# Optimization experiments

Measured on AMD Instinct MI355X. Metric: run time of the kernel, lower is better.

## Reference

```python
import jax, jax.numpy as jnp
import numpy as np

N_SRC = 1024     # source frames
N_TGT = 100000   # target pool frames
D = 1024         # WavLM layer-6 feature dim
K = 4            # neighbors


def setup_inputs() -> dict:
    key = jax.random.key(0)
    k1, k2 = jax.random.split(key)
    source_feats = jax.random.normal(k1, (N_SRC, D), dtype=jnp.float32)
    target_feats = jax.random.normal(k2, (N_TGT, D), dtype=jnp.float32)
    return {"source_feats": source_feats, "target_feats": target_feats, "k": K}


def reference(source_feats, target_feats, k):
    # Cosine distance kNN: smallest cosine distance == largest cosine similarity.
    s = source_feats / jnp.linalg.norm(source_feats, axis=-1, keepdims=True)
    t = target_feats / jnp.linalg.norm(target_feats, axis=-1, keepdims=True)
    sim = jnp.einsum('nd,md->nm', s, t)          # [N_SRC, N_TGT]
    _, idx = jax.lax.top_k(sim, k)               # [N_SRC, k] neighbor indices
    # Gather ORIGINAL (un-normalized) target rows and average over neighbors,
    # matching sklearn kneighbors + target_np[indices].mean(axis=0).
    gathered = target_feats[idx]                 # [N_SRC, k, D]
    return gathered.mean(axis=1)                 # [N_SRC, D]
```

## Files before the change

### kernel.cpp

```cpp
#include <hip/hip_runtime.h>
#include <hip/hip_bf16.h>
#include <float.h>

#define N_SRC 1024
#define N_TGT 100000
#define DIM   1024
#define KNN   4

#define BM 128
#define BN 256
#define BK 64
#define NKT (DIM / BK)
#define NMB 782
#define N_TGT2 (NMB * BM)
#define NSC (N_SRC / BN)
#define NBLK (NMB * NSC)
#define NSTRIP NMB
#define NCAND (NSTRIP * KNN)
#define RERANK 32

#define SRC_KT_B 65536ull
#define TGT_KT_B ((unsigned long long)N_TGT2 * 64ull)

typedef __attribute__((ext_vector_type(4))) float f32x4;
typedef __attribute__((ext_vector_type(4))) unsigned int u32x4;
typedef __attribute__((ext_vector_type(2))) long long i64x2;

__device__ __forceinline__ void gload16(const void* gp, void* lp) {
    __builtin_amdgcn_global_load_lds(
        (const __attribute__((address_space(1))) void*)gp,
        (__attribute__((address_space(3))) void*)lp, 16, 0, 0);
}

__device__ __forceinline__ unsigned int pk_fp8x4(float x0, float x1,
                                                 float x2, float x3) {
    int d = __builtin_amdgcn_cvt_pk_fp8_f32(x0, x1, 0, false);
    d     = __builtin_amdgcn_cvt_pk_fp8_f32(x2, x3, d, true);
    return (unsigned int)d;
}

__device__ __forceinline__ void ce_desc(float& v1, int& i1, float& v2, int& i2)
{
    bool sw = (v2 > v1) || (v2 == v1 && i2 < i1);
    float tv = sw ? v2 : v1; float uv = sw ? v1 : v2;
    int   ti = sw ? i2 : i1; int   ui = sw ? i1 : i2;
    v1 = tv; i1 = ti; v2 = uv; i2 = ui;
}

__global__ __launch_bounds__(256) void convert_src_kernel(
    const float* __restrict__ src, unsigned int* __restrict__ srcws)
{
    int gid = blockIdx.x * 256 + threadIdx.x;
    int kt  = gid >> 12;
    int rem = gid & 4095;
    int row = rem >> 2;
    int pos = rem & 3;
    int c   = pos ^ ((row >> 1) & 3);
    const float4* p0 = (const float4*)(src + (size_t)row * DIM + kt * BK + c * 8);
    const float4* p1 = (const float4*)(src + (size_t)row * DIM + kt * BK + 32 + c * 8);
    float4 a0 = p0[0], a1 = p0[1], b0 = p1[0], b1 = p1[1];
    u32x4 o = { pk_fp8x4(a0.x, a0.y, a0.z, a0.w),
                pk_fp8x4(a1.x, a1.y, a1.z, a1.w),
                pk_fp8x4(b0.x, b0.y, b0.z, b0.w),
                pk_fp8x4(b1.x, b1.y, b1.z, b1.w) };
    ((u32x4*)srcws)[gid] = o;
}

__global__ __launch_bounds__(256) void prep_tgt_kernel(
    const float* __restrict__ tgt, unsigned int* __restrict__ tgtbf,
    float* __restrict__ invnw)
{
    __shared__ float pn[16][17];
    const int t  = threadIdx.x;
    const int li = t & 15;
    const int kt = t >> 4;
    const int row = blockIdx.x * 16 + li;
    const bool valid = row < N_TGT;

    float4 v[16];
    if (valid) {
        const float4* p = (const float4*)(tgt + (size_t)row * DIM + kt * BK);
        #pragma unroll
        for (int i = 0; i < 16; ++i) v[i] = p[i];
    } else {
        #pragma unroll
        for (int i = 0; i < 16; ++i) v[i] = make_float4(0.f, 0.f, 0.f, 0.f);
    }
    float nsq = 0.f;
    #pragma unroll
    for (int i = 0; i < 16; ++i)
        nsq += v[i].x * v[i].x + v[i].y * v[i].y
             + v[i].z * v[i].z + v[i].w * v[i].w;

    u32x4* o = (u32x4*)((char*)tgtbf + (size_t)kt * TGT_KT_B
                        + (size_t)row * 64);
    const int f = (row >> 1) & 3;
    #pragma unroll
    for (int c = 0; c < 4; ++c) {
        float4 a0 = v[2 * c], a1 = v[2 * c + 1];
        float4 b0 = v[8 + 2 * c], b1 = v[8 + 2 * c + 1];
        o[c ^ f] = (u32x4){ pk_fp8x4(a0.x, a0.y, a0.z, a0.w),
                            pk_fp8x4(a1.x, a1.y, a1.z, a1.w),
                            pk_fp8x4(b0.x, b0.y, b0.z, b0.w),
                            pk_fp8x4(b1.x, b1.y, b1.z, b1.w) };
    }

    pn[li][kt] = nsq;
    __syncthreads();
    if (t < 16) {
        float s = 0.f;
        #pragma unroll
        for (int k = 0; k < 16; ++k) s += pn[t][k];
        int r2 = blockIdx.x * 16 + t;
        invnw[r2] = (r2 < N_TGT) ? 1.0f / sqrtf(s) : -1.0f;
    }
}

__global__ __launch_bounds__(512, 4) void gemm_topk_fp8_kernel(
    const void* __restrict__ tgtbf, const void* __restrict__ srcbf,
    const float* __restrict__ invnw,
    float* __restrict__ cand_val, int* __restrict__ cand_idx)
{
    __shared__ __align__(16) unsigned char As[2][BM][BK];
    __shared__ __align__(16) unsigned char Bs[2][BN][BK];
    __shared__ float invn_sh[BM];

    const int b = blockIdx.x;
    const int logical = (b & 7) * (NBLK / 8) + (b >> 3);
    const int mblk = logical >> 2;
    const int schk = logical & 3;
    const int m0 = mblk * BM;
    const int c0 = schk * BN;

    const int t = threadIdx.x;
    const int lane = t & 63;
    const int w = t >> 6;
    const int wm = w >> 2, wn = w & 3;
    const int g = lane >> 4, li = lane & 15;

    const char* tb_ = (const char*)tgtbf;
    const char* sb_ = (const char*)srcbf;

    f32x4 acc[4][4];
    #pragma unroll
    for (int i = 0; i < 4; ++i)
        #pragma unroll
        for (int j = 0; j < 4; ++j) acc[i][j] = (f32x4){0.f, 0.f, 0.f, 0.f};

    unsigned char *Ac = &As[0][0][0], *An = &As[1][0][0];
    unsigned char *Bc = &Bs[0][0][0], *Bn = &Bs[1][0][0];

    #define STAGE(Ab_, Bb_, kt_) do {                                         \
        const char* ga_ = tb_ + (size_t)(kt_) * TGT_KT_B + (size_t)m0 * 64    \
                          + (size_t)t * 16;                                   \
        gload16(ga_, (Ab_) + t * 16);                                         \
        const char* gb_ = sb_ + (size_t)(kt_) * SRC_KT_B + (size_t)c0 * 64    \
                          + (size_t)t * 16;                                   \
        gload16(gb_,        (Bb_) + t * 16);                                  \
        gload16(gb_ + 8192, (Bb_) + 8192 + t * 16);                           \
    } while (0)

    const int sl = (g ^ ((li >> 1) & 3)) * 16;

    #define READ_AB do {                                                      \
        _Pragma("unroll")                                                     \
        for (int mf = 0; mf < 4; ++mf)                                        \
            af[mf] = *(const i64x2*)(Ac + (wm * 64 + mf * 16 + li) * BK + sl);\
        _Pragma("unroll")                                                     \
        for (int nf = 0; nf < 4; ++nf)                                        \
            bf[nf] = *(const i64x2*)(Bc + (wn * 64 + nf * 16 + li) * BK + sl);\
    } while (0)

    #define DO_MFMA do {                                                      \
        _Pragma("unroll")                                                     \
        for (int mf = 0; mf < 4; ++mf)                                        \
            _Pragma("unroll")                                                 \
            for (int nf = 0; nf < 4; ++nf)                                    \
                acc[mf][nf] = __builtin_amdgcn_mfma_f32_16x16x32_fp8_fp8(     \
                    af[mf][0], bf[nf][0], acc[mf][nf], 0, 0, 0);              \
        _Pragma("unroll")                                                     \
        for (int mf = 0; mf < 4; ++mf)                                        \
            _Pragma("unroll")                                                 \
            for (int nf = 0; nf < 4; ++nf)                                    \
                acc[mf][nf] = __builtin_amdgcn_mfma_f32_16x16x32_fp8_fp8(     \
                    af[mf][1], bf[nf][1], acc[mf][nf], 0, 0, 0);              \
    } while (0)

    STAGE(Ac, Bc, 0);
    __syncthreads();

    for (int kt = 0; kt < NKT; ++kt) {
        if (kt + 1 < NKT) STAGE(An, Bn, kt + 1);
        i64x2 af[4], bf[4];
        READ_AB;
        DO_MFMA;
        __syncthreads();
        unsigned char* tmp_;
        tmp_ = Ac; Ac = An; An = tmp_;
        tmp_ = Bc; Bc = Bn; Bn = tmp_;
    }
    #undef STAGE
    #undef READ_AB
    #undef DO_MFMA

    float* scv = (float*)&As[0][0][0];
    int*   sci = (int*)&As[1][0][0];

    if (t < BM) invn_sh[t] = invnw[m0 + t];
    __syncthreads();

    float invr[4][4];
    #pragma unroll
    for (int mf = 0; mf < 4; ++mf)
        #pragma unroll
        for (int j = 0; j < 4; ++j)
            invr[mf][j] = invn_sh[wm * 64 + mf * 16 + g * 4 + j];

    #pragma unroll
    for (int nf = 0; nf < 4; ++nf) {
        const int col = wn * 64 + nf * 16 + li;
        float s[4][4];
        #pragma unroll
        for (int mf = 0; mf < 4; ++mf)
            #pragma unroll
            for (int j = 0; j < 4; ++j)
                s[mf][j] = (invr[mf][j] > 0.f) ? acc[mf][nf][j] * invr[mf][j]
                                               : -FLT_MAX;
        #pragma unroll
        for (int it = 0; it < KNN; ++it) {
            float bv = -FLT_MAX; int bli = 0;
            #pragma unroll
            for (int mf = 0; mf < 4; ++mf)
                #pragma unroll
                for (int j = 0; j < 4; ++j) {
                    int id = mf * 16 + g * 4 + j;
                    if (s[mf][j] > bv) { bv = s[mf][j]; bli = id; }
                }
            #pragma unroll
            for (int off = 16; off < 64; off <<= 1) {
                float ov = __shfl_xor(bv, off);
                int   oi = __shfl_xor(bli, off);
                if (ov > bv || (ov == bv && oi < bli)) { bv = ov; bli = oi; }
            }
            const int mfw = bli >> 4, gw = (bli >> 2) & 3, jw = bli & 3;
            if (g == gw) {
                #pragma unroll
                for (int mf = 0; mf < 4; ++mf)
                    #pragma unroll
                    for (int j = 0; j < 4; ++j)
                        if (mf == mfw && j == jw) s[mf][j] = -FLT_MAX;
            }
            if (g == it) {
                int o = (wm * BN + col) * KNN + it;
                scv[o] = bv;
                sci[o] = m0 + wm * 64 + bli;
            }
        }
    }
    __syncthreads();

    if (t < BN) {
        float v4[4] = { -FLT_MAX, -FLT_MAX, -FLT_MAX, -FLT_MAX };
        int   i4[4] = { 0x7fffffff, 0x7fffffff, 0x7fffffff, 0x7fffffff };
        #pragma unroll
        for (int q = 0; q < 8; ++q) {
            int o = ((q >> 2) * BN + t) * KNN + (q & 3);
            float v = scv[o]; int ix = sci[o];
            if (v > v4[3] || (v == v4[3] && ix < i4[3])) {
                v4[3] = v; i4[3] = ix;
                ce_desc(v4[2], i4[2], v4[3], i4[3]);
                ce_desc(v4[1], i4[1], v4[2], i4[2]);
                ce_desc(v4[0], i4[0], v4[1], i4[1]);
            }
        }
        size_t o = ((size_t)(c0 + t) * NSTRIP + mblk) * KNN;
        #pragma unroll
        for (int it = 0; it < KNN; ++it) {
            cand_val[o + it] = v4[it];
            cand_idx[o + it] = i4[it];
        }
    }
}

__global__ __launch_bounds__(256) void merge_rerank_kernel(
    const float* __restrict__ src, const float* __restrict__ tgt,
    const float* __restrict__ cand_val, const int* __restrict__ cand_idx,
    float* __restrict__ out)
{
    __shared__ float sv[NCAND];
    __shared__ float red_v[4];
    __shared__ int   red_p[4];
    __shared__ int   topi[RERANK];
    __shared__ float rsim[RERANK];
    __shared__ int   ridx[RERANK];
    __shared__ int   sel[KNN];

    const int row = blockIdx.x;
    const int t = threadIdx.x, lane = t & 63, w = t >> 6;
    const float* cv = cand_val + (size_t)row * NCAND;
    const int*   ci = cand_idx + (size_t)row * NCAND;

    for (int i = t; i < NCAND; i += 256) sv[i] = cv[i];
    __syncthreads();

    for (int it = 0; it < RERANK; ++it) {
        float bv = -FLT_MAX; int bp = 0;
        for (int i = t; i < NCAND; i += 256) {
            float v = sv[i];
            if (v > bv) { bv = v; bp = i; }
        }
        #pragma unroll
        for (int off = 1; off < 64; off <<= 1) {
            float ov = __shfl_xor(bv, off);
            int   op = __shfl_xor(bp, off);
            if (ov > bv || (ov == bv && op < bp)) { bv = ov; bp = op; }
        }
        if (lane == 0) { red_v[w] = bv; red_p[w] = bp; }
        __syncthreads();
        if (t == 0) {
            float Bv = red_v[0]; int Bp = red_p[0];
            for (int q = 1; q < 4; ++q)
                if (red_v[q] > Bv || (red_v[q] == Bv && red_p[q] < Bp)) {
                    Bv = red_v[q]; Bp = red_p[q];
                }
            topi[it] = ci[Bp];
            sv[Bp] = -FLT_MAX;
        }
        __syncthreads();
    }

    const float4* sp = (const float4*)(src + (size_t)row * DIM);
    #pragma unroll
    for (int q = 0; q < 8; ++q) {
        int cidx = topi[w + 4 * q];
        const float4* tp = (const float4*)(tgt + (size_t)cidx * DIM);
        float a = 0.f, nn = 0.f;
        #pragma unroll
        for (int p = 0; p < 4; ++p) {
            float4 x = sp[lane + 64 * p], y = tp[lane + 64 * p];
            a  = fmaf(x.x, y.x, a);  a  = fmaf(x.y, y.y, a);
            a  = fmaf(x.z, y.z, a);  a  = fmaf(x.w, y.w, a);
            nn = fmaf(y.x, y.x, nn); nn = fmaf(y.y, y.y, nn);
            nn = fmaf(y.z, y.z, nn); nn = fmaf(y.w, y.w, nn);
        }
        #pragma unroll
        for (int off = 1; off < 64; off <<= 1) {
            a  += __shfl_xor(a, off);
            nn += __shfl_xor(nn, off);
        }
        if (lane == 0) { rsim[w + 4 * q] = a / sqrtf(nn); ridx[w + 4 * q] = cidx; }
    }
    __syncthreads();

    if (w == 0) {
        float v = (lane < RERANK) ? rsim[lane] : -FLT_MAX;
        int  ix = (lane < RERANK) ? ridx[lane] : 0x7fffffff;
        #pragma unroll
        for (int it = 0; it < KNN; ++it) {
            float bv = v; int bix = ix;
            #pragma unroll
            for (int off = 1; off < 32; off <<= 1) {
                float ov = __shfl_xor(bv, off);
                int   oi = __shfl_xor(bix, off);
                if (ov > bv || (ov == bv && oi < bix)) { bv = ov; bix = oi; }
            }
            if (lane == 0) sel[it] = bix;
            if (ix == bix) v = -FLT_MAX;
        }
    }
    __syncthreads();

    const float4* g0 = (const float4*)(tgt + (size_t)sel[0] * DIM);
    const float4* g1 = (const float4*)(tgt + (size_t)sel[1] * DIM);
    const float4* g2 = (const float4*)(tgt + (size_t)sel[2] * DIM);
    const float4* g3 = (const float4*)(tgt + (size_t)sel[3] * DIM);
    float4* po = (float4*)(out + (size_t)row * DIM);
    float4 v0 = g0[t], v1 = g1[t], v2 = g2[t], v3 = g3[t];
    float4 rr;
    rr.x = (v0.x + v1.x + v2.x + v3.x) * 0.25f;
    rr.y = (v0.y + v1.y + v2.y + v3.y) * 0.25f;
    rr.z = (v0.z + v1.z + v2.z + v3.z) * 0.25f;
    rr.w = (v0.w + v1.w + v2.w + v3.w) * 0.25f;
    po[t] = rr;
}

extern "C" void kernel_launch(void* const* d_in, const int* in_sizes, int n_in,
                              void* d_out, int out_size, void* d_ws, size_t ws_size,
                              hipStream_t stream)
{
    const float* src = (const float*)d_in[0];
    const float* tgt = (const float*)d_in[1];
    float* out = (float*)d_out;

    const size_t SRCBF_B = 2097152;
    const size_t TGTBF_B = (size_t)N_TGT2 * 1024;
    const size_t INVN_B  = (size_t)N_TGT2 * 4;
    const size_t CV_B    = (size_t)N_SRC * NCAND * 4;

    char* p = (char*)d_ws;
    unsigned int* srcbf = (unsigned int*)p;
    unsigned int* tgtbf = (unsigned int*)(p + SRCBF_B);
    float* invnw    = (float*)(p + SRCBF_B + TGTBF_B);
    float* cand_val = (float*)(p + SRCBF_B + TGTBF_B + INVN_B);
    int*   cand_idx = (int*)(p + SRCBF_B + TGTBF_B + INVN_B + CV_B);

    convert_src_kernel<<<256, 256, 0, stream>>>(src, srcbf);
    prep_tgt_kernel<<<N_TGT2 / 16, 256, 0, stream>>>(tgt, tgtbf, invnw);
    gemm_topk_fp8_kernel<<<NBLK, 512, 0, stream>>>(tgtbf, srcbf, invnw,
                                                   cand_val, cand_idx);
    merge_rerank_kernel<<<N_SRC, 256, 0, stream>>>(src, tgt,
                                                   cand_val, cand_idx, out);
}
```

Baseline: 400.7 us.

## Load source FP8 fragments directly from global into registers, shrink block tile

The GEMM no longer stages the source (B) operand through LDS. Each wave reads its B fragments straight from global memory in a new fragment-friendly layout produced by the source conversion kernel. Only the target tile is double-buffered in LDS. The block shrinks to 256 threads with BN=128, so there are twice as many blocks and half the B footprint per block. This removes LDS traffic and barrier-bound staging for B, but it exposes global-load latency inside the MFMA loop because the B loads are not prefetched.

```diff
diff --git a/kernel.cpp b/kernel.cpp
--- a/kernel.cpp
+++ b/kernel.cpp
@@ -8,7 +8,7 @@
 #define KNN   4
 
 #define BM 128
-#define BN 256
+#define BN 128
 #define BK 64
 #define NKT (DIM / BK)
 #define NMB 782
@@ -53,9 +53,8 @@
     int gid = blockIdx.x * 256 + threadIdx.x;
     int kt  = gid >> 12;
     int rem = gid & 4095;
-    int row = rem >> 2;
-    int pos = rem & 3;
-    int c   = pos ^ ((row >> 1) & 3);
+    int c   = rem >> 10;
+    int row = rem & 1023;
     const float4* p0 = (const float4*)(src + (size_t)row * DIM + kt * BK + c * 8);
     const float4* p1 = (const float4*)(src + (size_t)row * DIM + kt * BK + 32 + c * 8);
     float4 a0 = p0[0], a1 = p0[1], b0 = p1[0], b1 = p1[1];
@@ -116,26 +115,25 @@
     }
 }
 
-__global__ __launch_bounds__(512, 4) void gemm_topk_fp8_kernel(
+__global__ __launch_bounds__(256, 4) void gemm_topk_fp8_kernel(
     const void* __restrict__ tgtbf, const void* __restrict__ srcbf,
     const float* __restrict__ invnw,
     float* __restrict__ cand_val, int* __restrict__ cand_idx)
 {
     __shared__ __align__(16) unsigned char As[2][BM][BK];
-    __shared__ __align__(16) unsigned char Bs[2][BN][BK];
     __shared__ float invn_sh[BM];
 
     const int b = blockIdx.x;
     const int logical = (b & 7) * (NBLK / 8) + (b >> 3);
-    const int mblk = logical >> 2;
-    const int schk = logical & 3;
+    const int mblk = logical >> 3;
+    const int schk = logical & 7;
     const int m0 = mblk * BM;
     const int c0 = schk * BN;
 
     const int t = threadIdx.x;
     const int lane = t & 63;
     const int w = t >> 6;
-    const int wm = w >> 2, wn = w & 3;
+    const int wm = w >> 1, wn = w & 1;
     const int g = lane >> 4, li = lane & 15;
 
     const char* tb_ = (const char*)tgtbf;
@@ -148,27 +146,28 @@
         for (int j = 0; j < 4; ++j) acc[i][j] = (f32x4){0.f, 0.f, 0.f, 0.f};
 
     unsigned char *Ac = &As[0][0][0], *An = &As[1][0][0];
-    unsigned char *Bc = &Bs[0][0][0], *Bn = &Bs[1][0][0];
-
-    #define STAGE(Ab_, Bb_, kt_) do {                                         \
-        const char* ga_ = tb_ + (size_t)(kt_) * TGT_KT_B + (size_t)m0 * 64    \
-                          + (size_t)t * 16;                                   \
-        gload16(ga_, (Ab_) + t * 16);                                         \
-        const char* gb_ = sb_ + (size_t)(kt_) * SRC_KT_B + (size_t)c0 * 64    \
-                          + (size_t)t * 16;                                   \
-        gload16(gb_,        (Bb_) + t * 16);                                  \
-        gload16(gb_ + 8192, (Bb_) + 8192 + t * 16);                           \
+
+    #define STAGE_A(Ab_, kt_) do {                                            \
+        const char* ga_ = tb_ + (size_t)(kt_) * TGT_KT_B + (size_t)m0 * 64;   \
+        gload16(ga_ + (size_t)t * 16,        (Ab_) + t * 16);                 \
+        gload16(ga_ + 4096 + (size_t)t * 16, (Ab_) + 4096 + t * 16);          \
     } while (0)
 
+    #define LOAD_B(kt_) do {                                                  \
+        const char* gb_ = sb_ + (size_t)(kt_) * SRC_KT_B + (size_t)g * 16384  \
+                          + (size_t)(c0 + wn * 64 + li) * 16;                 \
+        bf[0] = *(const i64x2*)(gb_ +   0);                                   \
+        bf[1] = *(const i64x2*)(gb_ + 256);                                   \
+        bf[2] = *(const i64x2*)(gb_ + 512);                                   \
+        bf[3] = *(const i64x2*)(gb_ + 768);                                   \
+    } while (0)
+
     const int sl = (g ^ ((li >> 1) & 3)) * 16;
 
-    #define READ_AB do {                                                      \
+    #define READ_A do {                                                       \
         _Pragma("unroll")                                                     \
         for (int mf = 0; mf < 4; ++mf)                                        \
             af[mf] = *(const i64x2*)(Ac + (wm * 64 + mf * 16 + li) * BK + sl);\
-        _Pragma("unroll")                                                     \
-        for (int nf = 0; nf < 4; ++nf)                                        \
-            bf[nf] = *(const i64x2*)(Bc + (wn * 64 + nf * 16 + li) * BK + sl);\
     } while (0)
 
     #define DO_MFMA do {                                                      \
@@ -186,21 +185,21 @@
                     af[mf][1], bf[nf][1], acc[mf][nf], 0, 0, 0);              \
     } while (0)
 
-    STAGE(Ac, Bc, 0);
+    STAGE_A(Ac, 0);
     __syncthreads();
 
     for (int kt = 0; kt < NKT; ++kt) {
-        if (kt + 1 < NKT) STAGE(An, Bn, kt + 1);
+        if (kt + 1 < NKT) STAGE_A(An, kt + 1);
         i64x2 af[4], bf[4];
-        READ_AB;
+        LOAD_B(kt);
+        READ_A;
         DO_MFMA;
         __syncthreads();
-        unsigned char* tmp_;
-        tmp_ = Ac; Ac = An; An = tmp_;
-        tmp_ = Bc; Bc = Bn; Bn = tmp_;
-    }
-    #undef STAGE
-    #undef READ_AB
+        unsigned char* tmp_ = Ac; Ac = An; An = tmp_;
+    }
+    #undef STAGE_A
+    #undef LOAD_B
+    #undef READ_A
     #undef DO_MFMA
 
     float* scv = (float*)&As[0][0][0];
@@ -406,7 +405,7 @@
 
     convert_src_kernel<<<256, 256, 0, stream>>>(src, srcbf);
     prep_tgt_kernel<<<N_TGT2 / 16, 256, 0, stream>>>(tgt, tgtbf, invnw);
-    gemm_topk_fp8_kernel<<<NBLK, 512, 0, stream>>>(tgtbf, srcbf, invnw,
+    gemm_topk_fp8_kernel<<<NBLK, 256, 0, stream>>>(tgtbf, srcbf, invnw,
                                                    cand_val, cand_idx);
     merge_rerank_kernel<<<N_SRC, 256, 0, stream>>>(src, tgt,
                                                    cand_val, cand_idx, out);
```

Result: faster. 380.2 us (-5.1%).
